# Optimization experiments

Hardware: AMD Instinct MI355X
Metric: run time of the kernel (lower is better)

The kernel has to match this reference:

```python
import jax, jax.numpy as jnp
import numpy as np

HIDDEN = 64
NUM_FEATURES = 32
BATCH = 64
SEQ = 2048


def setup_inputs() -> dict:
    key = jax.random.key(0)
    k_t, k_m, k_wr, k_br, k_wi, k_bi = jax.random.split(key, 6)
    # strictly increasing event times via cumsum of positive gaps
    gaps = jax.random.uniform(k_t, (BATCH, SEQ), minval=0.01, maxval=1.0)
    times = jnp.cumsum(gaps, axis=1)  # [B, T]
    marks = jax.random.uniform(k_m, (BATCH, SEQ, NUM_FEATURES))
    batch = jnp.concatenate([times[:, :, None], marks], axis=2)  # [B, T, 1+F]
    d_in = NUM_FEATURES + HIDDEN
    W_rec = jax.random.normal(k_wr, (d_in, 7 * HIDDEN)) / jnp.sqrt(d_in)
    b_rec = jnp.zeros((7 * HIDDEN,))
    W_int = jax.random.normal(k_wi, (HIDDEN, NUM_FEATURES)) / jnp.sqrt(HIDDEN)
    b_int = jnp.zeros((NUM_FEATURES,))
    return {"batch": batch, "W_rec": W_rec, "b_rec": b_rec,
            "W_int": W_int, "b_int": b_int}


def _ctlstm_forward(batch, W_rec, b_rec, W_int, b_int):
    times = batch[:, :, 0]          # [B, T]
    marks = batch[:, :, 1:]         # [B, T, F]
    B, T, _ = marks.shape
    # inter-event time for step t is times[t+1]-times[t]; last step has no decay
    dt = jnp.diff(times, axis=1)                                   # [B, T-1]
    dt = jnp.concatenate([dt, jnp.zeros((B, 1), dt.dtype)], 1)     # [B, T]

    def step(carry, inputs):
        h, c_decay, c_bar = carry
        x_t, dt_t = inputs          # [B, F], [B]
        z = jnp.concatenate([x_t, h], axis=1) @ W_rec + b_rec      # [B, 7H]
        i, f, g, o, i_bar, f_bar, delta = jnp.split(z, 7, axis=1)
        i = jax.nn.sigmoid(i)
        f = jax.nn.sigmoid(f)
        g = jnp.tanh(g)
        o = jax.nn.sigmoid(o)
        i_bar = jax.nn.sigmoid(i_bar)
        f_bar = jax.nn.sigmoid(f_bar)
        delta = jax.nn.softplus(delta)
        c = f * c_decay + i * g                    # (5a)
        c_bar_n = f_bar * c_bar + i_bar * g        # (5b)
        c_decay_n = c_bar_n + (c - c_bar_n) * jnp.exp(-delta * dt_t[:, None])  # (7)
        h_n = o * jnp.tanh(c_decay_n)              # (4b)
        intensity = jax.nn.softplus(h_n @ W_int + b_int)  # (4a)
        return (h_n, c_decay_n, c_bar_n), (o, c, c_bar_n, delta, intensity)

    h0 = jnp.zeros((B, HIDDEN), batch.dtype)
    carry0 = (h0, h0, h0)
    xs = (jnp.swapaxes(marks, 0, 1), jnp.swapaxes(dt, 0, 1))  # time-major
    _, (o, c, c_bar, delta, intensity) = jax.lax.scan(step, carry0, xs)
    tm = lambda a: jnp.swapaxes(a, 0, 1)  # [T,B,*] -> [B,T,*]
    # intensity defined only for t < T-1 (last decay step is skipped in original)
    return (tm(o), tm(c), tm(c_bar), tm(delta), tm(intensity)[:, :-1, :])


def reference(batch, W_rec, b_rec, W_int, b_int):
    return _ctlstm_forward(batch, W_rec, b_rec, W_int, b_int)
```

## Files before the change

### kernel.cpp

```cpp
#include <hip/hip_runtime.h>
#include <hip/hip_bf16.h>

#define BATCHN 64
#define SEQ    2048
#define HID    64
#define NF     32
#define DIN    96
#define G7     448
#define CH     33

using bf16 = __hip_bfloat16;

__device__ __forceinline__ float b2f(bf16 v) { return __bfloat162float(v); }

__device__ __forceinline__ float ldin(const void* p, size_t i, bool f32) {
    return f32 ? ((const float*)p)[i] : b2f(((const bf16*)p)[i]);
}

__device__ __forceinline__ float fast_rcp(float x) { return __builtin_amdgcn_rcpf(x); }
__device__ __forceinline__ float sigmoid_f(float x) {
    return fast_rcp(1.0f + __expf(-x));
}
__device__ __forceinline__ float tanh_f(float x) {
    float e = __expf(2.0f * x);
    return 1.0f - 2.0f * fast_rcp(e + 1.0f);
}
__device__ __forceinline__ float softplus_f(float x) {
    float e = __expf(-fabsf(x));
    return fmaxf(x, 0.0f) + __logf(1.0f + e);
}

__global__ void detect_dtype(const void* batch, int* flag) {
    if (threadIdx.x != 0 || blockIdx.x != 0) return;
    const float* bf = (const float*)batch;
    bool mono = true;
    float prev = bf[0];
    if (!(prev > 0.004f && prev < 1.3f)) mono = false;
    for (int t = 1; t < 16 && mono; ++t) {
        float cur = bf[(size_t)t * CH];
        if (!(cur > prev && (cur - prev) < 1.3f)) mono = false;
        prev = cur;
    }
    *flag = mono ? 1 : 0;
}

__global__ __launch_bounds__(G7) void xproj_gemm(
    const void* __restrict__ batch, const void* __restrict__ W_rec,
    const void* __restrict__ b_rec, float* __restrict__ xz,
    const int* __restrict__ flag)
{
    const bool f32 = *flag != 0;
    const int tid = threadIdx.x;
    const size_t base = (size_t)blockIdx.x * 64;

    float wx[NF];
    if (f32) {
        const float* W = (const float*)W_rec;
#pragma unroll
        for (int k = 0; k < NF; ++k) wx[k] = W[(size_t)k * G7 + tid];
    } else {
        const bf16* W = (const bf16*)W_rec;
#pragma unroll
        for (int k = 0; k < NF; ++k) wx[k] = b2f(W[(size_t)k * G7 + tid]);
    }
    const float bias = ldin(b_rec, tid, f32);

    __shared__ __align__(16) float s_x[64][NF];
    for (int i = tid; i < 64 * NF; i += G7) {
        const int r = i >> 5, k = i & 31;
        s_x[r][k] = ldin(batch, (base + r) * CH + 1 + k, f32);
    }
    __syncthreads();

    for (int r = 0; r < 64; ++r) {
        const float4* xv = (const float4*)s_x[r];
        float a0 = 0.f, a1 = 0.f, a2 = 0.f, a3 = 0.f;
#pragma unroll
        for (int k4 = 0; k4 < NF / 4; ++k4) {
            float4 v = xv[k4];
            a0 = fmaf(v.x, wx[4 * k4 + 0], a0);
            a1 = fmaf(v.y, wx[4 * k4 + 1], a1);
            a2 = fmaf(v.z, wx[4 * k4 + 2], a2);
            a3 = fmaf(v.w, wx[4 * k4 + 3], a3);
        }
        xz[(base + r) * G7 + tid] = bias + ((a0 + a1) + (a2 + a3));
    }
}

__global__ __launch_bounds__(G7, 2) void ctlstm_rec_xz(
    const void* __restrict__ batch, const void* __restrict__ W_rec,
    const float* __restrict__ xz, float* __restrict__ out,
    float* __restrict__ h_ws, const int* __restrict__ flag)
{
    const bool f32 = *flag != 0;
    const int tid  = threadIdx.x;
    const int wave = tid >> 6;
    const int lane = tid & 63;
    const int b    = blockIdx.x;
    const size_t bT = (size_t)b * SEQ;

    float* out_o  = out;
    float* out_c  = out + (size_t)BATCHN * SEQ * HID;
    float* out_cb = out + 2 * (size_t)BATCHN * SEQ * HID;
    float* out_dl = out + 3 * (size_t)BATCHN * SEQ * HID;

    __shared__ __align__(16) float s_h[7][HID];
    __shared__ float s_act[2][G7];
    __shared__ float s_times[SEQ];

    float wh[HID];
    if (f32) {
        const float* W = (const float*)W_rec;
#pragma unroll
        for (int k = 0; k < HID; ++k) wh[k] = W[(size_t)(NF + k) * G7 + tid];
    } else {
        const bf16* W = (const bf16*)W_rec;
#pragma unroll
        for (int k = 0; k < HID; ++k) wh[k] = b2f(W[(size_t)(NF + k) * G7 + tid]);
    }

    for (int i = tid; i < SEQ; i += G7)
        s_times[i] = ldin(batch, (bT + i) * CH, f32);
    s_h[wave][lane] = 0.0f;
    float c_decay = 0.0f, c_bar = 0.0f;

    float xz_cur = xz[bT * G7 + tid];
    float xz_next = 0.0f;
    __syncthreads();

    for (int t = 0; t < SEQ; ++t) {
        const float4* hv = (const float4*)s_h[wave];
        float a0 = 0.f, a1 = 0.f, a2 = 0.f, a3 = 0.f;
#pragma unroll
        for (int k4 = 0; k4 < HID / 4; ++k4) {
            float4 v = hv[k4];
            a0 = fmaf(v.x, wh[4 * k4 + 0], a0);
            a1 = fmaf(v.y, wh[4 * k4 + 1], a1);
            a2 = fmaf(v.z, wh[4 * k4 + 2], a2);
            a3 = fmaf(v.w, wh[4 * k4 + 3], a3);
        }
        const float z = xz_cur + ((a0 + a1) + (a2 + a3));

        float act;
        if (wave == 2)      act = tanh_f(z);
        else if (wave == 6) act = softplus_f(z);
        else                act = sigmoid_f(z);
        s_act[t & 1][tid] = act;
        __syncthreads();

        if (t + 1 < SEQ) xz_next = xz[(bT + t + 1) * G7 + tid];

        const float ig = s_act[t & 1][lane];
        const float fg = s_act[t & 1][HID + lane];
        const float gg = s_act[t & 1][2 * HID + lane];
        const float og = s_act[t & 1][3 * HID + lane];
        const float ib = s_act[t & 1][4 * HID + lane];
        const float fb = s_act[t & 1][5 * HID + lane];
        const float dl = s_act[t & 1][6 * HID + lane];
        const float c  = fg * c_decay + ig * gg;
        const float cbn = fb * c_bar + ib * gg;
        float dt = (t + 1 < SEQ) ? (s_times[t + 1] - s_times[t]) : 0.0f;
        dt = fmaxf(dt, 0.0f);
        const float cd = cbn + (c - cbn) * __expf(-dl * dt);
        const float h  = og * tanh_f(cd);
        c_decay = cd;
        c_bar   = cbn;
        s_h[wave][lane] = h;

        const size_t idx = (bT + t) * HID + lane;
        if (wave == 0) out_c[idx]  = c;
        else if (wave == 1) out_cb[idx] = cbn;
        else if (wave == 2) h_ws[idx]   = h;
        else if (wave == 3) out_o[idx]  = act;
        else if (wave == 6) out_dl[idx] = act;
        xz_cur = xz_next;
    }
}

__global__ __launch_bounds__(G7, 2) void ctlstm_rec(
    const void* __restrict__ batch, const void* __restrict__ W_rec,
    const void* __restrict__ b_rec, float* __restrict__ out,
    float* __restrict__ h_ws, int use_ws, const int* __restrict__ flag)
{
    const bool f32 = flag ? (*flag != 0) : true;
    const int tid = threadIdx.x;
    const int b   = blockIdx.x;
    const size_t bT = (size_t)b * SEQ;

    float* out_o  = out;
    float* out_c  = out + (size_t)BATCHN * SEQ * HID;
    float* out_cb = out + 2 * (size_t)BATCHN * SEQ * HID;
    float* out_dl = out + 3 * (size_t)BATCHN * SEQ * HID;

    __shared__ __align__(16) float s_in[DIN];
    __shared__ float s_act[G7];
    __shared__ float s_times[SEQ];

    float wcol[DIN];
    if (f32) {
        const float* W = (const float*)W_rec;
#pragma unroll
        for (int k = 0; k < DIN; ++k) wcol[k] = W[(size_t)k * G7 + tid];
    } else {
        const bf16* W = (const bf16*)W_rec;
#pragma unroll
        for (int k = 0; k < DIN; ++k) wcol[k] = b2f(W[(size_t)k * G7 + tid]);
    }
    const float bias = ldin(b_rec, tid, f32);

    for (int i = tid; i < SEQ; i += G7)
        s_times[i] = ldin(batch, (bT + i) * CH, f32);

    if (tid >= NF && tid < DIN) s_in[tid] = 0.0f;
    float c_decay = 0.0f, c_bar = 0.0f;

    float xpref = 0.0f;
    if (tid < NF) xpref = ldin(batch, bT * CH + 1 + tid, f32);
    __syncthreads();

    const int gate = tid >> 6;
    const int lane = tid & 63;

    for (int t = 0; t < SEQ; ++t) {
        if (tid < NF) s_in[tid] = xpref;
        __syncthreads();

        const float4* sv = (const float4*)s_in;
        float a0 = 0.f, a1 = 0.f, a2 = 0.f, a3 = 0.f;
#pragma unroll
        for (int k4 = 0; k4 < DIN / 4; ++k4) {
            float4 v = sv[k4];
            a0 = fmaf(v.x, wcol[4 * k4 + 0], a0);
            a1 = fmaf(v.y, wcol[4 * k4 + 1], a1);
            a2 = fmaf(v.z, wcol[4 * k4 + 2], a2);
            a3 = fmaf(v.w, wcol[4 * k4 + 3], a3);
        }
        const float z = bias + ((a0 + a1) + (a2 + a3));

        float act;
        if (gate == 2)      act = tanh_f(z);
        else if (gate == 6) act = softplus_f(z);
        else                act = sigmoid_f(z);
        s_act[tid] = act;

        const size_t oidx = (bT + t) * HID + lane;
        if (gate == 3) out_o[oidx]  = act;
        if (gate == 6) out_dl[oidx] = act;
        __syncthreads();

        if (tid < HID) {
            const float ig = s_act[tid];
            const float fg = s_act[HID + tid];
            const float gg = s_act[2 * HID + tid];
            const float og = s_act[3 * HID + tid];
            const float ib = s_act[4 * HID + tid];
            const float fb = s_act[5 * HID + tid];
            const float dl = s_act[6 * HID + tid];
            const float c  = fg * c_decay + ig * gg;
            const float cb = fb * c_bar + ib * gg;
            float dt = (t + 1 < SEQ) ? (s_times[t + 1] - s_times[t]) : 0.0f;
            dt = fmaxf(dt, 0.0f);
            const float cd = cb + (c - cb) * __expf(-dl * dt);
            const float h  = og * tanh_f(cd);
            c_decay = cd;
            c_bar   = cb;
            s_in[NF + tid] = h;
            const size_t idx = (bT + t) * HID + tid;
            out_c[idx]  = c;
            out_cb[idx] = cb;
            if (use_ws) h_ws[idx] = h;
        }
        if (tid < NF && t + 1 < SEQ)
            xpref = ldin(batch, (bT + t + 1) * CH + 1 + tid, f32);
    }
}

__global__ __launch_bounds__(256) void intensity_ws(
    const float* __restrict__ h_ws, const void* __restrict__ W_int,
    const void* __restrict__ b_int, float* __restrict__ out_int,
    const int* __restrict__ flag)
{
    const bool f32 = flag ? (*flag != 0) : true;
    __shared__ float s_w[HID * NF];
    __shared__ float s_b[NF];
    const int tx = threadIdx.x, ty = threadIdx.y;
    const int lt = ty * 32 + tx;
    for (int k = lt; k < HID * NF; k += 256) s_w[k] = ldin(W_int, k, f32);
    if (lt < NF) s_b[lt] = ldin(b_int, lt, f32);
    __syncthreads();

    const int b = blockIdx.y;
    const int t = blockIdx.x * 8 + ty;
    if (t >= SEQ - 1) return;
    const float* hr = h_ws + ((size_t)b * SEQ + t) * HID;
    float acc = s_b[tx];
#pragma unroll
    for (int k = 0; k < HID; ++k) acc = fmaf(hr[k], s_w[k * NF + tx], acc);
    out_int[((size_t)b * (SEQ - 1) + t) * NF + tx] = softplus_f(acc);
}

__global__ __launch_bounds__(256) void intensity_rec(
    const void* __restrict__ batch, const float* __restrict__ out,
    const void* __restrict__ W_int, const void* __restrict__ b_int,
    float* __restrict__ out_int, const int* __restrict__ flag)
{
    const bool f32 = flag ? (*flag != 0) : true;
    __shared__ float s_w[HID * NF];
    __shared__ float s_b[NF];
    __shared__ float s_h[8][HID];
    const int tx = threadIdx.x, ty = threadIdx.y;
    const int lt = ty * 32 + tx;
    for (int k = lt; k < HID * NF; k += 256) s_w[k] = ldin(W_int, k, f32);
    if (lt < NF) s_b[lt] = ldin(b_int, lt, f32);

    const int b  = blockIdx.y;
    const int t0 = blockIdx.x * 8;
    const float* out_o  = out;
    const float* out_c  = out + (size_t)BATCHN * SEQ * HID;
    const float* out_cb = out + 2 * (size_t)BATCHN * SEQ * HID;
    const float* out_dl = out + 3 * (size_t)BATCHN * SEQ * HID;

#pragma unroll
    for (int r = 0; r < 2; ++r) {
        const int flat = lt + r * 256;
        const int row  = flat >> 6;
        const int k    = flat & 63;
        const int t    = t0 + row;
        if (t < SEQ - 1) {
            const size_t idx = ((size_t)b * SEQ + t) * HID + k;
            const float og = out_o[idx];
            const float c  = out_c[idx];
            const float cb = out_cb[idx];
            const float dl = out_dl[idx];
            const float t_a = ldin(batch, ((size_t)b * SEQ + t) * CH, f32);
            const float t_b = ldin(batch, ((size_t)b * SEQ + t + 1) * CH, f32);
            const float dt = fmaxf(t_b - t_a, 0.0f);
            const float cd = cb + (c - cb) * __expf(-dl * dt);
            s_h[row][k] = og * tanh_f(cd);
        }
    }
    __syncthreads();
    const int t = t0 + ty;
    if (t >= SEQ - 1) return;
    float acc = s_b[tx];
#pragma unroll
    for (int k = 0; k < HID; ++k) acc = fmaf(s_h[ty][k], s_w[k * NF + tx], acc);
    out_int[((size_t)b * (SEQ - 1) + t) * NF + tx] = softplus_f(acc);
}

extern "C" void kernel_launch(void* const* d_in, const int* in_sizes, int n_in,
                              void* d_out, int out_size, void* d_ws, size_t ws_size,
                              hipStream_t stream) {
    const void* batch = d_in[0];
    const void* W_rec = d_in[1];
    const void* b_rec = d_in[2];
    const void* W_int = d_in[3];
    const void* b_int = d_in[4];
    float* out = (float*)d_out;

    const size_t hb  = (size_t)BATCHN * SEQ * HID * sizeof(float);
    const size_t xzb = (size_t)BATCHN * SEQ * G7  * sizeof(float);
    int*   flag = (ws_size >= 4) ? (int*)d_ws : nullptr;
    float* h_ws = (float*)((char*)d_ws + 256);
    float* xz   = (float*)((char*)d_ws + 256 + hb);
    const int have_h  = (ws_size >= 256 + hb) ? 1 : 0;
    const int have_xz = (ws_size >= 256 + hb + xzb) ? 1 : 0;

    if (flag) detect_dtype<<<1, 64, 0, stream>>>(batch, flag);

    float* out_int = out + 4 * (size_t)BATCHN * SEQ * HID;

    if (have_xz) {
        xproj_gemm<<<(BATCHN * SEQ) / 64, G7, 0, stream>>>(batch, W_rec, b_rec, xz, flag);
        ctlstm_rec_xz<<<BATCHN, G7, 0, stream>>>(batch, W_rec, xz, out, h_ws, flag);
        intensity_ws<<<dim3((SEQ - 1 + 7) / 8, BATCHN), dim3(32, 8), 0, stream>>>(
            h_ws, W_int, b_int, out_int, flag);
    } else if (have_h) {
        ctlstm_rec<<<BATCHN, G7, 0, stream>>>(batch, W_rec, b_rec, out, h_ws, 1, flag);
        intensity_ws<<<dim3((SEQ - 1 + 7) / 8, BATCHN), dim3(32, 8), 0, stream>>>(
            h_ws, W_int, b_int, out_int, flag);
    } else {
        ctlstm_rec<<<BATCHN, G7, 0, stream>>>(batch, W_rec, b_rec, out, h_ws, 0, flag);
        intensity_rec<<<dim3((SEQ - 1 + 7) / 8, BATCHN), dim3(32, 8), 0, stream>>>(
            batch, out, W_int, b_int, out_int, flag);
    }
}
```

Measured before the change: 1.804 ms.

## Shrink recurrent kernel to 4 waves with readlane h broadcast

The recurrent kernel now runs 256 threads per batch row instead of 448. Waves 0-2 each compute two gate columns and wave 3 computes one, with the recurrent weights held as float2 registers. The hidden state stays in a register and is broadcast through readlane, which removes the shared-memory h buffer. A raw s_barrier with an explicit lgkmcnt wait replaces __syncthreads, and the xz prefetch now runs two steps ahead. Fewer waves means cheaper barriers, but each wave does twice the FMA work on the serial critical path, and readlane broadcasts use the scalar path. Also, every wave except 0-2 (here only wave 3) writes both o and delta outputs, and waves 0, 1 and 2 compute o/dl but don't write them.

```diff
diff --git a/kernel.cpp b/kernel.cpp
--- a/kernel.cpp
+++ b/kernel.cpp
@@ -8,6 +8,7 @@
 #define DIN    96
 #define G7     448
 #define CH     33
+#define REC_T  256
 
 using bf16 = __hip_bfloat16;
 
@@ -28,6 +29,10 @@
 __device__ __forceinline__ float softplus_f(float x) {
     float e = __expf(-fabsf(x));
     return fmaxf(x, 0.0f) + __logf(1.0f + e);
+}
+
+__device__ __forceinline__ float rl(float v, int lane) {
+    return __uint_as_float(__builtin_amdgcn_readlane(__float_as_uint(v), lane));
 }
 
 __global__ void detect_dtype(const void* batch, int* flag) {
@@ -87,7 +92,7 @@
     }
 }
 
-__global__ __launch_bounds__(G7, 2) void ctlstm_rec_xz(
+__global__ __launch_bounds__(REC_T, 1) void ctlstm_rec_xz4(
     const void* __restrict__ batch, const void* __restrict__ W_rec,
     const float* __restrict__ xz, float* __restrict__ out,
     float* __restrict__ h_ws, const int* __restrict__ flag)
@@ -104,60 +109,82 @@
     float* out_cb = out + 2 * (size_t)BATCHN * SEQ * HID;
     float* out_dl = out + 3 * (size_t)BATCHN * SEQ * HID;
 
-    __shared__ __align__(16) float s_h[7][HID];
     __shared__ float s_act[2][G7];
     __shared__ float s_times[SEQ];
 
-    float wh[HID];
+    const int c0 = tid;
+    const int c1 = (wave < 3) ? tid + 256 : tid;
+
+    float2 wh[HID];
     if (f32) {
         const float* W = (const float*)W_rec;
 #pragma unroll
-        for (int k = 0; k < HID; ++k) wh[k] = W[(size_t)(NF + k) * G7 + tid];
+        for (int k = 0; k < HID; ++k) {
+            wh[k].x = W[(size_t)(NF + k) * G7 + c0];
+            wh[k].y = W[(size_t)(NF + k) * G7 + c1];
+        }
     } else {
         const bf16* W = (const bf16*)W_rec;
 #pragma unroll
-        for (int k = 0; k < HID; ++k) wh[k] = b2f(W[(size_t)(NF + k) * G7 + tid]);
-    }
-
-    for (int i = tid; i < SEQ; i += G7)
+        for (int k = 0; k < HID; ++k) {
+            wh[k].x = b2f(W[(size_t)(NF + k) * G7 + c0]);
+            wh[k].y = b2f(W[(size_t)(NF + k) * G7 + c1]);
+        }
+    }
+
+    for (int i = tid; i < SEQ; i += REC_T)
         s_times[i] = ldin(batch, (bT + i) * CH, f32);
-    s_h[wave][lane] = 0.0f;
-    float c_decay = 0.0f, c_bar = 0.0f;
-
-    float xz_cur = xz[bT * G7 + tid];
-    float xz_next = 0.0f;
+
+    float h_reg = 0.0f, c_decay = 0.0f, c_bar = 0.0f;
+
+    float xa0 = xz[bT * G7 + c0];
+    float xb0 = xz[bT * G7 + c1];
+    float xa1 = xz[(bT + 1) * G7 + c0];
+    float xb1 = xz[(bT + 1) * G7 + c1];
     __syncthreads();
 
     for (int t = 0; t < SEQ; ++t) {
-        const float4* hv = (const float4*)s_h[wave];
-        float a0 = 0.f, a1 = 0.f, a2 = 0.f, a3 = 0.f;
-#pragma unroll
-        for (int k4 = 0; k4 < HID / 4; ++k4) {
-            float4 v = hv[k4];
-            a0 = fmaf(v.x, wh[4 * k4 + 0], a0);
-            a1 = fmaf(v.y, wh[4 * k4 + 1], a1);
-            a2 = fmaf(v.z, wh[4 * k4 + 2], a2);
-            a3 = fmaf(v.w, wh[4 * k4 + 3], a3);
-        }
-        const float z = xz_cur + ((a0 + a1) + (a2 + a3));
-
-        float act;
-        if (wave == 2)      act = tanh_f(z);
-        else if (wave == 6) act = softplus_f(z);
-        else                act = sigmoid_f(z);
-        s_act[t & 1][tid] = act;
-        __syncthreads();
-
-        if (t + 1 < SEQ) xz_next = xz[(bT + t + 1) * G7 + tid];
-
-        const float ig = s_act[t & 1][lane];
-        const float fg = s_act[t & 1][HID + lane];
-        const float gg = s_act[t & 1][2 * HID + lane];
-        const float og = s_act[t & 1][3 * HID + lane];
-        const float ib = s_act[t & 1][4 * HID + lane];
-        const float fb = s_act[t & 1][5 * HID + lane];
-        const float dl = s_act[t & 1][6 * HID + lane];
-        const float c  = fg * c_decay + ig * gg;
+        float xa2 = 0.0f, xb2 = 0.0f;
+        if (t + 2 < SEQ) {
+            xa2 = xz[(bT + t + 2) * G7 + c0];
+            xb2 = xz[(bT + t + 2) * G7 + c1];
+        }
+
+        float a0x = 0.f, a1x = 0.f, a2x = 0.f, a3x = 0.f;
+        float a0y = 0.f, a1y = 0.f, a2y = 0.f, a3y = 0.f;
+#pragma unroll
+        for (int k = 0; k < HID; k += 4) {
+            const float h0 = rl(h_reg, k + 0);
+            const float h1 = rl(h_reg, k + 1);
+            const float h2 = rl(h_reg, k + 2);
+            const float h3 = rl(h_reg, k + 3);
+            a0x = fmaf(h0, wh[k + 0].x, a0x); a0y = fmaf(h0, wh[k + 0].y, a0y);
+            a1x = fmaf(h1, wh[k + 1].x, a1x); a1y = fmaf(h1, wh[k + 1].y, a1y);
+            a2x = fmaf(h2, wh[k + 2].x, a2x); a2y = fmaf(h2, wh[k + 2].y, a2y);
+            a3x = fmaf(h3, wh[k + 3].x, a3x); a3y = fmaf(h3, wh[k + 3].y, a3y);
+        }
+        const float z0 = xa0 + ((a0x + a1x) + (a2x + a3x));
+        const float z1 = xb0 + ((a0y + a1y) + (a2y + a3y));
+
+        const float act0 = (wave == 2) ? tanh_f(z0) : sigmoid_f(z0);
+        const float act1 = (wave == 2) ? softplus_f(z1) : sigmoid_f(z1);
+
+        const int p = t & 1;
+        s_act[p][c0] = act0;
+        if (wave < 3) s_act[p][c1] = act1;
+
+        asm volatile("s_waitcnt lgkmcnt(0)" ::: "memory");
+        __builtin_amdgcn_s_barrier();
+        __builtin_amdgcn_sched_barrier(0);
+
+        const float ig = s_act[p][lane];
+        const float fg = s_act[p][HID + lane];
+        const float gg = s_act[p][2 * HID + lane];
+        const float og = s_act[p][3 * HID + lane];
+        const float ib = s_act[p][4 * HID + lane];
+        const float fb = s_act[p][5 * HID + lane];
+        const float dl = s_act[p][6 * HID + lane];
+        const float c   = fg * c_decay + ig * gg;
         const float cbn = fb * c_bar + ib * gg;
         float dt = (t + 1 < SEQ) ? (s_times[t + 1] - s_times[t]) : 0.0f;
         dt = fmaxf(dt, 0.0f);
@@ -165,15 +192,15 @@
         const float h  = og * tanh_f(cd);
         c_decay = cd;
         c_bar   = cbn;
-        s_h[wave][lane] = h;
+        h_reg   = h;
 
         const size_t idx = (bT + t) * HID + lane;
-        if (wave == 0) out_c[idx]  = c;
+        if (wave == 0)      out_c[idx]  = c;
         else if (wave == 1) out_cb[idx] = cbn;
         else if (wave == 2) h_ws[idx]   = h;
-        else if (wave == 3) out_o[idx]  = act;
-        else if (wave == 6) out_dl[idx] = act;
-        xz_cur = xz_next;
+        else                { out_o[idx] = og; out_dl[idx] = dl; }
+
+        xa0 = xa1; xb0 = xb1; xa1 = xa2; xb1 = xb2;
     }
 }
 
@@ -372,7 +399,7 @@
 
     if (have_xz) {
         xproj_gemm<<<(BATCHN * SEQ) / 64, G7, 0, stream>>>(batch, W_rec, b_rec, xz, flag);
-        ctlstm_rec_xz<<<BATCHN, G7, 0, stream>>>(batch, W_rec, xz, out, h_ws, flag);
+        ctlstm_rec_xz4<<<BATCHN, REC_T, 0, stream>>>(batch, W_rec, xz, out, h_ws, flag);
         intensity_ws<<<dim3((SEQ - 1 + 7) / 8, BATCHN), dim3(32, 8), 0, stream>>>(
             h_ws, W_int, b_int, out_int, flag);
     } else if (have_h) {
```

Result: no change. 1.788 ms (-0.9%).
